# Kernel optimization log

Measured on AMD Instinct MI355X. Metric: run time of the kernel, lower is better.

## Reference

```python
import jax, jax.numpy as jnp
import numpy as np

B, T, H = 2048, 64, 64
N_LANE, N_PHASE = 8, 8
# phase -> (lane1, lane2) from phase_startLane_mapping (lanes indexed 0..7)
PHASE_LANES = np.array([[1, 3], [0, 2], [5, 7], [4, 6], [0, 1], [2, 3], [4, 5], [6, 7]])
# pairwise (i, j) with i != j, row-major i then j (matches the python double loop)
I_IDX = np.repeat(np.arange(N_PHASE), N_PHASE - 1).reshape(N_PHASE, N_PHASE - 1)
J_IDX = np.array([[j for j in range(N_PHASE) if j != i] for i in range(N_PHASE)])
# per-lane history gather: [idx, idx+phase_dim, idx+phase_dim+vehicle_dim]
HIST_IDX = np.stack([np.arange(N_LANE), np.arange(N_LANE) + 8, np.arange(N_LANE) + 16], axis=-1)


def setup_inputs():
    key = jax.random.key(0)
    ks = jax.random.split(key, 16)
    ph_bits = jax.random.randint(ks[0], (B, 8), 0, 2).astype(jnp.float32)
    veh_cnt = jax.random.uniform(ks[1], (B, 8)) * 10.0
    feature_input = jnp.concatenate([ph_bits, veh_cnt], axis=-1)  # [B,16]
    history_input = jax.random.uniform(ks[2], (B, T, 24))
    relation = jax.random.randint(ks[3], (8, 7), 0, 2).astype(jnp.int32)
    s = 0.2
    p = {}
    p['emb_phase'] = jax.random.normal(ks[4], (2, 4)) * s
    p['Wv'] = jax.random.normal(ks[5], (4, 1)) * s
    p['bv'] = jnp.zeros((4,))
    p['Wh'] = jax.random.normal(ks[6], (4, 3)) * s
    p['bh'] = jnp.zeros((4,))
    p['Wih'] = jax.random.normal(ks[7], (3 * H, 4)) * s
    p['Whh'] = jax.random.normal(ks[8], (3 * H, H)) * s
    p['bih'] = jnp.zeros((3 * H,))
    p['bhh'] = jnp.zeros((3 * H,))
    p['Wl'] = jax.random.normal(ks[9], (16, 8 + H)) * s
    p['bl'] = jnp.zeros((16,))
    p['emb_const'] = jax.random.normal(ks[10], (2, 4)) * s
    p['Wcf'] = jax.random.normal(ks[11], (20, 32)) * s
    p['bcf'] = jnp.zeros((20,))
    p['Wcc'] = jax.random.normal(ks[12], (20, 4)) * s
    p['bcc'] = jnp.zeros((20,))
    p['Wcm'] = jax.random.normal(ks[13], (20, 20)) * s
    p['bcm'] = jnp.zeros((20,))
    p['Wfin'] = jax.random.normal(ks[14], (1, 20)) * s
    p['bfin'] = jnp.zeros((1,))
    return {'feature_input': feature_input, 'history_input': history_input, 'relation': relation, **p}


def _gru_last(x, Wih, Whh, bih, bhh):
    # x: [N, T, 4] -> final hidden state [N, H]; PyTorch GRU gate order (r, z, n)
    n = x.shape[0]
    h_dim = Whh.shape[1]

    def step(hprev, xt):
        gi = xt @ Wih.T + bih          # [N, 3H]
        gh = hprev @ Whh.T + bhh       # [N, 3H]
        i_r, i_z, i_n = jnp.split(gi, 3, axis=-1)
        h_r, h_z, h_n = jnp.split(gh, 3, axis=-1)
        r = jax.nn.sigmoid(i_r + h_r)
        z = jax.nn.sigmoid(i_z + h_z)
        cand = jnp.tanh(i_n + r * h_n)
        hnew = (1 - z) * cand + z * hprev
        return hnew, None

    h0 = jnp.zeros((n, h_dim), x.dtype)
    hT, _ = jax.lax.scan(step, h0, jnp.swapaxes(x, 0, 1))
    return hT


def _forward(feature_input, history_input, relation, emb_phase, Wv, bv, Wh, bh,
             Wih, Whh, bih, bhh, Wl, bl, emb_const, Wcf, bcf, Wcc, bcc, Wcm, bcm, Wfin, bfin):
    b = feature_input.shape[0]
    phase_ids = jax.lax.stop_gradient(feature_input[:, :8]).astype(jnp.int32)
    veh_raw = feature_input[:, 8:]                                     # [B,8]
    ph = jax.nn.sigmoid(emb_phase[phase_ids])                          # [B,8,4]
    veh = jax.nn.sigmoid(veh_raw[..., None] * Wv[:, 0] + bv)           # Linear(1,4): [B,8,4]
    hist = history_input[:, :, HIST_IDX]                               # [B,T,8,3]
    hist = jax.nn.sigmoid(jnp.einsum('btlc,oc->btlo', hist, Wh) + bh)  # [B,T,8,4]
    x = jnp.swapaxes(hist, 1, 2).reshape(b * N_LANE, T, 4)
    hidden = _gru_last(x, Wih, Whh, bih, bhh).reshape(b, N_LANE, H)
    lane_feat = jnp.concatenate([veh, ph, hidden], axis=-1)            # [B,8,8+H]
    line = jax.nn.relu(lane_feat @ Wl.T + bl)                          # [B,8,16]
    pp = line[:, PHASE_LANES].sum(axis=2)                              # phase pressure [B,8,16]
    fm = jnp.concatenate([pp[:, I_IDX], pp[:, J_IDX]], axis=-1)        # [B,8,7,32]
    ce = emb_const[relation]                                           # [8,7,4]
    xf = jax.nn.relu(jnp.einsum('bpqc,oc->bpqo', fm, Wcf) + bcf)       # 1x1 conv [B,8,7,20]
    yc = jax.nn.relu(ce @ Wcc.T + bcc)                                 # [8,7,20] (broadcast over B)
    z = jax.nn.relu(jnp.einsum('bpqc,oc->bpqo', xf * yc, Wcm) + bcm)
    z = jnp.einsum('bpqc,oc->bpqo', z, Wfin) + bfin                    # [B,8,7,1]
    return z.sum(axis=2)[..., 0]                                       # sum over competing phases -> [B,8]


def reference(feature_input, history_input, relation, emb_phase, Wv, bv, Wh, bh,
              Wih, Whh, bih, bhh, Wl, bl, emb_const, Wcf, bcf, Wcc, bcc, Wcm, bcm, Wfin, bfin):
    return _forward(feature_input, history_input, relation, emb_phase, Wv, bv, Wh, bh,
                    Wih, Whh, bih, bhh, Wl, bl, emb_const, Wcf, bcf, Wcc, bcc, Wcm, bcm, Wfin, bfin)
```

## Files before the change

### kernel.cpp

```cpp
#include <hip/hip_runtime.h>

typedef unsigned short u16;
typedef unsigned int   u32;

typedef __attribute__((ext_vector_type(8))) short short8;
typedef __attribute__((ext_vector_type(4))) float f32x4;

union Frag { u32 u[4]; short8 s; };

__device__ __forceinline__ u32 fbits(float f){ union{float f;u32 u;}x; x.f=f; return x.u; }
__device__ __forceinline__ float bitsf(u32 u){ union{u32 u;float f;}x; x.u=u; return x.f; }
__device__ __forceinline__ u32 pack_trunc(float a, float b){
    return __builtin_amdgcn_perm(fbits(b), fbits(a), 0x07060302u);
}
__device__ __forceinline__ u32 bf16_rne(float a){
    u32 u = fbits(a); return (u + 0x7FFFu + ((u >> 16) & 1u)) >> 16;
}
__device__ __forceinline__ u32 pack_rne(float a, float b){
    return bf16_rne(a) | (bf16_rne(b) << 16);
}
__device__ __forceinline__ float sigmoidf_(float x){
    return __builtin_amdgcn_rcpf(1.0f + __expf(-x));
}
__device__ __forceinline__ float tanhf_(float x){
    return 1.0f - 2.0f * __builtin_amdgcn_rcpf(__expf(2.0f * x) + 1.0f);
}

struct __align__(16) SharedMem {
    union {
        struct {
            u16   hh[2][16][72];
            u16   hl[2][16][72];
            float uall[64][16][4];
            float wih[768];
        } lp;
        struct {
            float wl[1152];
            float bl[16];
            float wcf[640];
            float bcf[20];
            float wcc[80];
            float bcc[20];
            float wcm[400];
            float bcm[20];
            float wfin[20];
            float bfin;
            float line[2][128];
            float pp[2][128];
        } tl;
    };
    float h[16 * 68];
};

__global__ __launch_bounds__(256, 4)
void FRAPRQ_fused_kernel(
    const float* __restrict__ feat,
    const float* __restrict__ hist,
    const int*   __restrict__ relation,
    const float* __restrict__ emb_phase,
    const float* __restrict__ Wv,
    const float* __restrict__ bv,
    const float* __restrict__ Wh,
    const float* __restrict__ bh,
    const float* __restrict__ Wih,
    const float* __restrict__ Whh,
    const float* __restrict__ bih,
    const float* __restrict__ bhh,
    const float* __restrict__ Wl,
    const float* __restrict__ bl,
    const float* __restrict__ emb_const,
    const float* __restrict__ Wcf,
    const float* __restrict__ bcf,
    const float* __restrict__ Wcc,
    const float* __restrict__ bcc,
    const float* __restrict__ Wcm,
    const float* __restrict__ bcm,
    const float* __restrict__ Wfin,
    const float* __restrict__ bfin,
    float* __restrict__ out)
{
    __shared__ SharedMem sm;
    const int tid  = threadIdx.x;
    const int w    = tid >> 6;
    const int lane = tid & 63;
    const int sq   = lane & 15;
    const int q    = lane >> 4;
    const int b_base = blockIdx.x * 2;

    for (int i = tid; i < 768; i += 256) sm.lp.wih[i] = Wih[i];
    {
        u32* z = (u32*)&sm.lp.hh[0][0][0];
        #pragma unroll 1
        for (int i = tid; i < 2304; i += 256) z[i] = 0u;
    }

    {
        const int s  = tid & 15;
        const int c  = (tid >> 4) & 3;
        const int tg = tid >> 6;
        const int bs_ = b_base + (s >> 3), ls_ = s & 7;
        const float* hbp = hist + (size_t)bs_ * 1536;
        const float w0 = Wh[c*3+0], w1 = Wh[c*3+1], w2 = Wh[c*3+2], bc = bh[c];
        #pragma unroll
        for (int i = 0; i < 16; ++i){
            const int t = tg * 16 + i;
            const float x0 = hbp[t*24 + ls_];
            const float x1 = hbp[t*24 + ls_ + 8];
            const float x2 = hbp[t*24 + ls_ + 16];
            sm.lp.uall[t][s][c] = sigmoidf_(fmaf(w0, x0, fmaf(w1, x1, fmaf(w2, x2, bc))));
        }
    }

    Frag ahi[6], alo[6];
    #pragma unroll
    for (int g3 = 0; g3 < 3; ++g3){
        #pragma unroll
        for (int c = 0; c < 2; ++c){
            const int idx = g3 * 2 + c;
            const float* wp = Whh + (64 * g3 + 16 * w + sq) * 64 + 32 * c + 8 * q;
            const float4 fA = *(const float4*)wp;
            const float4 fB = *(const float4*)(wp + 4);
            const float f[8] = {fA.x, fA.y, fA.z, fA.w, fB.x, fB.y, fB.z, fB.w};
            #pragma unroll
            for (int p = 0; p < 4; ++p){
                const u32 hi = pack_rne(f[2*p], f[2*p+1]);
                ahi[idx].u[p] = hi;
                const float l0 = f[2*p]   - bitsf((hi & 0xFFFFu) << 16);
                const float l1 = f[2*p+1] - bitsf(hi & 0xFFFF0000u);
                alo[idx].u[p] = pack_rne(l0, l1);
            }
        }
    }

    float bR[4], bZ[4], bNi[4], bNh[4];
    #pragma unroll
    for (int r = 0; r < 4; ++r){
        const int j = 16 * w + 4 * q + r;
        bR[r]  = bih[j]       + bhh[j];
        bZ[r]  = bih[64 + j]  + bhh[64 + j];
        bNi[r] = bih[128 + j];
        bNh[r] = bhh[128 + j];
    }

    float hreg[4] = {0.f, 0.f, 0.f, 0.f};

    __syncthreads();

    #pragma unroll 1
    for (int t = 0; t < 64; ++t){
        const int rb = t & 1;

        const short8 bh0 = *(const short8*)&sm.lp.hh[rb][sq][8 * q];
        const short8 bl0 = *(const short8*)&sm.lp.hl[rb][sq][8 * q];
        const short8 bh1 = *(const short8*)&sm.lp.hh[rb][sq][32 + 8 * q];
        const short8 bl1 = *(const short8*)&sm.lp.hl[rb][sq][32 + 8 * q];

        const float4 u4 = *(const float4*)&sm.lp.uall[t][sq][0];
        f32x4 aR, aZ, aN;
        float giN[4];
        #pragma unroll
        for (int r = 0; r < 4; ++r){
            const int j = 16 * w + 4 * q + r;
            const float4 wr = *(const float4*)&sm.lp.wih[j * 4];
            const float4 wz = *(const float4*)&sm.lp.wih[(64 + j) * 4];
            const float4 wn = *(const float4*)&sm.lp.wih[(128 + j) * 4];
            aR[r]  = fmaf(wr.x,u4.x, fmaf(wr.y,u4.y, fmaf(wr.z,u4.z, fmaf(wr.w,u4.w, bR[r]))));
            aZ[r]  = fmaf(wz.x,u4.x, fmaf(wz.y,u4.y, fmaf(wz.z,u4.z, fmaf(wz.w,u4.w, bZ[r]))));
            giN[r] = fmaf(wn.x,u4.x, fmaf(wn.y,u4.y, fmaf(wn.z,u4.z, fmaf(wn.w,u4.w, bNi[r]))));
            aN[r]  = bNh[r];
        }

        #define MM3(acc, i, BH, BL) \
            acc = __builtin_amdgcn_mfma_f32_16x16x32_bf16(ahi[i].s, BH, acc, 0, 0, 0); \
            acc = __builtin_amdgcn_mfma_f32_16x16x32_bf16(ahi[i].s, BL, acc, 0, 0, 0); \
            acc = __builtin_amdgcn_mfma_f32_16x16x32_bf16(alo[i].s, BH, acc, 0, 0, 0);
        MM3(aR, 0, bh0, bl0)
        MM3(aZ, 2, bh0, bl0)
        MM3(aN, 4, bh0, bl0)
        MM3(aR, 1, bh1, bl1)
        MM3(aZ, 3, bh1, bl1)
        MM3(aN, 5, bh1, bl1)
        #undef MM3

        float hn4[4];
        #pragma unroll
        for (int r = 0; r < 4; ++r){
            const float rr   = sigmoidf_(aR[r]);
            const float zz   = sigmoidf_(aZ[r]);
            const float cand = tanhf_(fmaf(rr, aN[r], giN[r]));
            const float hn   = fmaf(zz, hreg[r] - cand, cand);
            hreg[r] = hn;
            hn4[r] = hn;
        }

        {
            const u32 hi0 = pack_trunc(hn4[0], hn4[1]);
            const u32 hi1 = pack_trunc(hn4[2], hn4[3]);
            const float l0 = hn4[0] - bitsf((hi0 & 0xFFFFu) << 16);
            const float l1 = hn4[1] - bitsf(hi0 & 0xFFFF0000u);
            const float l2 = hn4[2] - bitsf((hi1 & 0xFFFFu) << 16);
            const float l3 = hn4[3] - bitsf(hi1 & 0xFFFF0000u);
            const u32 lo0 = pack_trunc(l0, l1);
            const u32 lo1 = pack_trunc(l2, l3);
            const int wb = rb ^ 1;
            *(uint2*)&sm.lp.hh[wb][sq][16 * w + 4 * q] = make_uint2(hi0, hi1);
            *(uint2*)&sm.lp.hl[wb][sq][16 * w + 4 * q] = make_uint2(lo0, lo1);
        }

        __syncthreads();
    }

    {
        const float4 hv = make_float4(hreg[0], hreg[1], hreg[2], hreg[3]);
        *(float4*)&sm.h[sq * 68 + 16 * w + 4 * q] = hv;
    }

    for (int i = tid; i < 1152; i += 256) sm.tl.wl[i]  = Wl[i];
    for (int i = tid; i <  640; i += 256) sm.tl.wcf[i] = Wcf[i];
    for (int i = tid; i <  400; i += 256) sm.tl.wcm[i] = Wcm[i];
    if (tid < 80) sm.tl.wcc[tid] = Wcc[tid];
    if (tid < 20){
        sm.tl.bcf[tid]  = bcf[tid];
        sm.tl.bcc[tid]  = bcc[tid];
        sm.tl.bcm[tid]  = bcm[tid];
        sm.tl.wfin[tid] = Wfin[tid];
    }
    if (tid < 16) sm.tl.bl[tid] = bl[tid];
    if (tid == 0) sm.tl.bfin = bfin[0];
    __syncthreads();

    {
        const int g    = w & 1;
        const int half = w >> 1;
        const int b    = b_base + g;
        const int l = lane >> 3, o = lane & 7;
        float fv[8];
        const float vraw = feat[b * 16 + 8 + l];
        const int   bit  = ((int)feat[b * 16 + l]) & 1;
        #pragma unroll
        for (int c = 0; c < 4; ++c){
            fv[c]     = sigmoidf_(fmaf(vraw, Wv[c], bv[c]));
            fv[4 + c] = sigmoidf_(emb_phase[bit * 4 + c]);
        }
        const float* hrow = &sm.h[(g * 8 + l) * 68];
        const int oo = o + half * 8;
        float acc = sm.tl.bl[oo];
        #pragma unroll
        for (int f = 0; f < 8; ++f) acc = fmaf(fv[f], sm.tl.wl[oo * 72 + f], acc);
        for (int k = 0; k < 64; ++k) acc = fmaf(hrow[k], sm.tl.wl[oo * 72 + 8 + k], acc);
        sm.tl.line[g][l * 16 + oo] = fmaxf(acc, 0.0f);
    }
    __syncthreads();

    if (w < 2){
        const int g = w;
        const int b = b_base + g;
        {
            const int p = lane >> 3, o = lane & 7;
            const int l0 = (0x64204501u >> (p * 4)) & 15;
            const int l1 = (0x75316723u >> (p * 4)) & 15;
            sm.tl.pp[g][p * 16 + o]     = sm.tl.line[g][l0 * 16 + o]     + sm.tl.line[g][l1 * 16 + o];
            sm.tl.pp[g][p * 16 + o + 8] = sm.tl.line[g][l0 * 16 + o + 8] + sm.tl.line[g][l1 * 16 + o + 8];
        }
        __builtin_amdgcn_wave_barrier();
        if (lane < 56){
            const int p  = lane / 7;
            const int qi = lane - p * 7;
            const int jl = qi + (qi >= p ? 1 : 0);
            float fmv[32];
            #pragma unroll
            for (int f = 0; f < 16; ++f){
                fmv[f]      = sm.tl.pp[g][p  * 16 + f];
                fmv[16 + f] = sm.tl.pp[g][jl * 16 + f];
            }
            const int rel = relation[p * 7 + qi] & 1;
            float ce[4];
            #pragma unroll
            for (int c = 0; c < 4; ++c) ce[c] = emb_const[rel * 4 + c];
            float m[20];
            for (int o = 0; o < 20; ++o){
                float xf = sm.tl.bcf[o];
                #pragma unroll
                for (int f = 0; f < 32; ++f) xf = fmaf(fmv[f], sm.tl.wcf[o * 32 + f], xf);
                float yc = sm.tl.bcc[o];
                #pragma unroll
                for (int c = 0; c < 4; ++c) yc = fmaf(ce[c], sm.tl.wcc[o * 4 + c], yc);
                m[o] = fmaxf(xf, 0.0f) * fmaxf(yc, 0.0f);
            }
            float fin = sm.tl.bfin;
            for (int o = 0; o < 20; ++o){
                float zz = sm.tl.bcm[o];
                #pragma unroll
                for (int c = 0; c < 20; ++c) zz = fmaf(m[c], sm.tl.wcm[o * 20 + c], zz);
                fin = fmaf(fmaxf(zz, 0.0f), sm.tl.wfin[o], fin);
            }
            sm.tl.line[g][lane] = fin;
        }
        __builtin_amdgcn_wave_barrier();
        if (lane < 8){
            float acc = 0.0f;
            #pragma unroll
            for (int qq = 0; qq < 7; ++qq) acc += sm.tl.line[g][lane * 7 + qq];
            out[b * 8 + lane] = acc;
        }
    }
}

extern "C" void kernel_launch(void* const* d_in, const int* in_sizes, int n_in,
                              void* d_out, int out_size, void* d_ws, size_t ws_size,
                              hipStream_t stream) {
    (void)n_in; (void)d_ws; (void)ws_size; (void)out_size;
    const float* feat      = (const float*)d_in[0];
    const float* hist      = (const float*)d_in[1];
    const int*   relation  = (const int*)d_in[2];
    const float* emb_phase = (const float*)d_in[3];
    const float* Wv        = (const float*)d_in[4];
    const float* bv        = (const float*)d_in[5];
    const float* Wh        = (const float*)d_in[6];
    const float* bh        = (const float*)d_in[7];
    const float* Wih       = (const float*)d_in[8];
    const float* Whh       = (const float*)d_in[9];
    const float* bih       = (const float*)d_in[10];
    const float* bhh       = (const float*)d_in[11];
    const float* Wl        = (const float*)d_in[12];
    const float* bl        = (const float*)d_in[13];
    const float* emb_const = (const float*)d_in[14];
    const float* Wcf       = (const float*)d_in[15];
    const float* bcf       = (const float*)d_in[16];
    const float* Wcc       = (const float*)d_in[17];
    const float* bcc       = (const float*)d_in[18];
    const float* Wcm       = (const float*)d_in[19];
    const float* bcm       = (const float*)d_in[20];
    const float* Wfin      = (const float*)d_in[21];
    const float* bfin      = (const float*)d_in[22];
    float* out = (float*)d_out;

    const int B = in_sizes[0] / 16;
    const int nblocks = B / 2;
    FRAPRQ_fused_kernel<<<nblocks, 256, 0, stream>>>(
        feat, hist, relation, emb_phase, Wv, bv, Wh, bh, Wih, Whh, bih, bhh,
        Wl, bl, emb_const, Wcf, bcf, Wcc, bcc, Wcm, bcm, Wfin, bfin, out);
}
```

Before: 225.6 us.

## Move GRU input projection onto MFMA and prescale gates for exp2

Stores the per-timestep sigmoid inputs as split-bf16 hi/lo pairs and folds the Wih input projection into the MFMA accumulation chain, using zero-padded A/B fragments. This replaces the per-step scalar FMA loop and its LDS weight reads. Whh, Wih and the biases are prescaled by -log2e or 2·log2e so the gates can call exp2 directly without a multiply. This adds extra MFMAs per step and lane-select logic for the fragments. Split-bf16 rounding of the input projection slightly changes numerics.

```diff
diff --git a/kernel.cpp b/kernel.cpp
--- a/kernel.cpp
+++ b/kernel.cpp
@@ -22,17 +22,15 @@
 __device__ __forceinline__ float sigmoidf_(float x){
     return __builtin_amdgcn_rcpf(1.0f + __expf(-x));
 }
-__device__ __forceinline__ float tanhf_(float x){
-    return 1.0f - 2.0f * __builtin_amdgcn_rcpf(__expf(2.0f * x) + 1.0f);
-}
+
+#define LOG2E 1.4426950408889634f
 
 struct __align__(16) SharedMem {
     union {
         struct {
-            u16   hh[2][16][72];
-            u16   hl[2][16][72];
-            float uall[64][16][4];
-            float wih[768];
+            u16 hh[2][16][72];
+            u16 hl[2][16][72];
+            u32 uallp[64][16][4];
         } lp;
         struct {
             float wl[1152];
@@ -87,7 +85,6 @@
     const int q    = lane >> 4;
     const int b_base = blockIdx.x * 2;
 
-    for (int i = tid; i < 768; i += 256) sm.lp.wih[i] = Wih[i];
     {
         u32* z = (u32*)&sm.lp.hh[0][0][0];
         #pragma unroll 1
@@ -96,20 +93,37 @@
 
     {
         const int s  = tid & 15;
-        const int c  = (tid >> 4) & 3;
-        const int tg = tid >> 6;
+        const int tg = tid >> 4;
         const int bs_ = b_base + (s >> 3), ls_ = s & 7;
         const float* hbp = hist + (size_t)bs_ * 1536;
-        const float w0 = Wh[c*3+0], w1 = Wh[c*3+1], w2 = Wh[c*3+2], bc = bh[c];
-        #pragma unroll
-        for (int i = 0; i < 16; ++i){
-            const int t = tg * 16 + i;
+        float whc[12], bhc[4];
+        #pragma unroll
+        for (int c = 0; c < 4; ++c){
+            whc[c*3+0] = Wh[c*3+0]; whc[c*3+1] = Wh[c*3+1]; whc[c*3+2] = Wh[c*3+2];
+            bhc[c] = bh[c];
+        }
+        #pragma unroll
+        for (int i = 0; i < 4; ++i){
+            const int t = tg * 4 + i;
             const float x0 = hbp[t*24 + ls_];
             const float x1 = hbp[t*24 + ls_ + 8];
             const float x2 = hbp[t*24 + ls_ + 16];
-            sm.lp.uall[t][s][c] = sigmoidf_(fmaf(w0, x0, fmaf(w1, x1, fmaf(w2, x2, bc))));
-        }
-    }
+            float u_[4];
+            #pragma unroll
+            for (int c = 0; c < 4; ++c)
+                u_[c] = sigmoidf_(fmaf(whc[c*3], x0, fmaf(whc[c*3+1], x1, fmaf(whc[c*3+2], x2, bhc[c]))));
+            const u32 uh01 = pack_rne(u_[0], u_[1]);
+            const u32 uh23 = pack_rne(u_[2], u_[3]);
+            const float l0 = u_[0] - bitsf((uh01 & 0xFFFFu) << 16);
+            const float l1 = u_[1] - bitsf(uh01 & 0xFFFF0000u);
+            const float l2 = u_[2] - bitsf((uh23 & 0xFFFFu) << 16);
+            const float l3 = u_[3] - bitsf(uh23 & 0xFFFF0000u);
+            *(uint4*)&sm.lp.uallp[t][s][0] =
+                make_uint4(uh01, uh23, pack_rne(l0, l1), pack_rne(l2, l3));
+        }
+    }
+
+    const float gsc[3] = { -LOG2E, -LOG2E, 2.0f * LOG2E };
 
     Frag ahi[6], alo[6];
     #pragma unroll
@@ -120,7 +134,9 @@
             const float* wp = Whh + (64 * g3 + 16 * w + sq) * 64 + 32 * c + 8 * q;
             const float4 fA = *(const float4*)wp;
             const float4 fB = *(const float4*)(wp + 4);
-            const float f[8] = {fA.x, fA.y, fA.z, fA.w, fB.x, fB.y, fB.z, fB.w};
+            const float s3 = gsc[g3];
+            const float f[8] = {fA.x*s3, fA.y*s3, fA.z*s3, fA.w*s3,
+                                fB.x*s3, fB.y*s3, fB.z*s3, fB.w*s3};
             #pragma unroll
             for (int p = 0; p < 4; ++p){
                 const u32 hi = pack_rne(f[2*p], f[2*p+1]);
@@ -132,19 +148,45 @@
         }
     }
 
-    float bR[4], bZ[4], bNi[4], bNh[4];
+    Frag auR, auZ, auN;
+    {
+        Frag* dst[3] = { &auR, &auZ, &auN };
+        #pragma unroll
+        for (int g3 = 0; g3 < 3; ++g3){
+            const int row = 64 * g3 + 16 * w + sq;
+            const float4 wv4 = *(const float4*)&Wih[row * 4];
+            const float s3 = gsc[g3];
+            const float v0 = wv4.x*s3, v1 = wv4.y*s3, v2 = wv4.z*s3, v3 = wv4.w*s3;
+            const u32 whi01 = pack_rne(v0, v1);
+            const u32 whi23 = pack_rne(v2, v3);
+            const float r0 = v0 - bitsf((whi01 & 0xFFFFu) << 16);
+            const float r1 = v1 - bitsf(whi01 & 0xFFFF0000u);
+            const float r2 = v2 - bitsf((whi23 & 0xFFFFu) << 16);
+            const float r3 = v3 - bitsf(whi23 & 0xFFFF0000u);
+            const u32 wlo01 = pack_rne(r0, r1);
+            const u32 wlo23 = pack_rne(r2, r3);
+            dst[g3]->u[0] = (q <= 1) ? whi01 : 0u;
+            dst[g3]->u[1] = (q <= 1) ? whi23 : 0u;
+            dst[g3]->u[2] = (q == 0) ? wlo01 : 0u;
+            dst[g3]->u[3] = (q == 0) ? wlo23 : 0u;
+        }
+    }
+
+    f32x4 bR4, bZ4, bNh4, bNi4;
     #pragma unroll
     for (int r = 0; r < 4; ++r){
         const int j = 16 * w + 4 * q + r;
-        bR[r]  = bih[j]       + bhh[j];
-        bZ[r]  = bih[64 + j]  + bhh[64 + j];
-        bNi[r] = bih[128 + j];
-        bNh[r] = bhh[128 + j];
+        bR4[r]  = -LOG2E * (bih[j]       + bhh[j]);
+        bZ4[r]  = -LOG2E * (bih[64 + j]  + bhh[64 + j]);
+        bNi4[r] = 2.0f * LOG2E * bih[128 + j];
+        bNh4[r] = 2.0f * LOG2E * bhh[128 + j];
     }
 
     float hreg[4] = {0.f, 0.f, 0.f, 0.f};
 
     __syncthreads();
+
+    #define MFMA_(A,B,C) __builtin_amdgcn_mfma_f32_16x16x32_bf16(A, B, C, 0, 0, 0)
 
     #pragma unroll 1
     for (int t = 0; t < 64; ++t){
@@ -154,40 +196,32 @@
         const short8 bl0 = *(const short8*)&sm.lp.hl[rb][sq][8 * q];
         const short8 bh1 = *(const short8*)&sm.lp.hh[rb][sq][32 + 8 * q];
         const short8 bl1 = *(const short8*)&sm.lp.hl[rb][sq][32 + 8 * q];
-
-        const float4 u4 = *(const float4*)&sm.lp.uall[t][sq][0];
-        f32x4 aR, aZ, aN;
-        float giN[4];
+        const uint4 uv = *(const uint4*)&sm.lp.uallp[t][sq][0];
+        Frag bu;
+        bu.u[0] = (q == 0) ? uv.x : ((q == 1) ? uv.z : 0u);
+        bu.u[1] = (q == 0) ? uv.y : ((q == 1) ? uv.w : 0u);
+        bu.u[2] = (q == 0) ? uv.x : 0u;
+        bu.u[3] = (q == 0) ? uv.y : 0u;
+
+        f32x4 aR = MFMA_(auR.s, bu.s, bR4);
+        aR = MFMA_(ahi[0].s, bh0, aR); aR = MFMA_(ahi[0].s, bl0, aR); aR = MFMA_(alo[0].s, bh0, aR);
+        aR = MFMA_(ahi[1].s, bh1, aR); aR = MFMA_(ahi[1].s, bl1, aR); aR = MFMA_(alo[1].s, bh1, aR);
+        f32x4 aZ = MFMA_(auZ.s, bu.s, bZ4);
+        aZ = MFMA_(ahi[2].s, bh0, aZ); aZ = MFMA_(ahi[2].s, bl0, aZ); aZ = MFMA_(alo[2].s, bh0, aZ);
+        aZ = MFMA_(ahi[3].s, bh1, aZ); aZ = MFMA_(ahi[3].s, bl1, aZ); aZ = MFMA_(alo[3].s, bh1, aZ);
+        f32x4 aN = MFMA_(ahi[4].s, bh0, bNh4);
+        aN = MFMA_(ahi[4].s, bl0, aN); aN = MFMA_(alo[4].s, bh0, aN);
+        aN = MFMA_(ahi[5].s, bh1, aN); aN = MFMA_(ahi[5].s, bl1, aN); aN = MFMA_(alo[5].s, bh1, aN);
+        f32x4 gN = MFMA_(auN.s, bu.s, bNi4);
+
+        float hn4[4];
         #pragma unroll
         for (int r = 0; r < 4; ++r){
-            const int j = 16 * w + 4 * q + r;
-            const float4 wr = *(const float4*)&sm.lp.wih[j * 4];
-            const float4 wz = *(const float4*)&sm.lp.wih[(64 + j) * 4];
-            const float4 wn = *(const float4*)&sm.lp.wih[(128 + j) * 4];
-            aR[r]  = fmaf(wr.x,u4.x, fmaf(wr.y,u4.y, fmaf(wr.z,u4.z, fmaf(wr.w,u4.w, bR[r]))));
-            aZ[r]  = fmaf(wz.x,u4.x, fmaf(wz.y,u4.y, fmaf(wz.z,u4.z, fmaf(wz.w,u4.w, bZ[r]))));
-            giN[r] = fmaf(wn.x,u4.x, fmaf(wn.y,u4.y, fmaf(wn.z,u4.z, fmaf(wn.w,u4.w, bNi[r]))));
-            aN[r]  = bNh[r];
-        }
-
-        #define MM3(acc, i, BH, BL) \
-            acc = __builtin_amdgcn_mfma_f32_16x16x32_bf16(ahi[i].s, BH, acc, 0, 0, 0); \
-            acc = __builtin_amdgcn_mfma_f32_16x16x32_bf16(ahi[i].s, BL, acc, 0, 0, 0); \
-            acc = __builtin_amdgcn_mfma_f32_16x16x32_bf16(alo[i].s, BH, acc, 0, 0, 0);
-        MM3(aR, 0, bh0, bl0)
-        MM3(aZ, 2, bh0, bl0)
-        MM3(aN, 4, bh0, bl0)
-        MM3(aR, 1, bh1, bl1)
-        MM3(aZ, 3, bh1, bl1)
-        MM3(aN, 5, bh1, bl1)
-        #undef MM3
-
-        float hn4[4];
-        #pragma unroll
-        for (int r = 0; r < 4; ++r){
-            const float rr   = sigmoidf_(aR[r]);
-            const float zz   = sigmoidf_(aZ[r]);
-            const float cand = tanhf_(fmaf(rr, aN[r], giN[r]));
+            const float rr   = __builtin_amdgcn_rcpf(1.0f + __builtin_amdgcn_exp2f(aR[r]));
+            const float zz   = __builtin_amdgcn_rcpf(1.0f + __builtin_amdgcn_exp2f(aZ[r]));
+            const float y    = fmaf(rr, aN[r], gN[r]);
+            const float cand = fmaf(-2.0f,
+                __builtin_amdgcn_rcpf(__builtin_amdgcn_exp2f(y) + 1.0f), 1.0f);
             const float hn   = fmaf(zz, hreg[r] - cand, cand);
             hreg[r] = hn;
             hn4[r] = hn;
@@ -209,6 +243,7 @@
 
         __syncthreads();
     }
+    #undef MFMA_
 
     {
         const float4 hv = make_float4(hreg[0], hreg[1], hreg[2], hreg[3]);
```

Measured after the change: 200.1 us. -11.3%, faster.
